# Kernel optimization log

Measured on AMD Instinct MI355X. Metric: run time of the kernel, lower is better.

The kernel has to match this reference:

```python
import jax, jax.numpy as jnp
import numpy as np

B, H, S, D = 4, 16, 2048, 128

def setup_inputs() -> dict:
    key = jax.random.key(0)
    kq, kk, kv = jax.random.split(key, 3)
    query = jax.random.normal(kq, (B, H, S, D), dtype=jnp.float32)
    k = jax.random.normal(kk, (B, H, S, D), dtype=jnp.float32)
    v = jax.random.normal(kv, (B, H, S, D), dtype=jnp.float32)
    # causal mask: True = masked (not attended), broadcastable to (B,H,S,S)
    mask = jnp.triu(jnp.ones((S, S), dtype=bool), k=1)[None, None, :, :]
    return {"query": query, "key": k, "value": v, "mask": mask}

def reference(query, key, value, mask):
    d_k = query.shape[-1]
    scale = 1.0 / np.sqrt(d_k).astype(np.float32)
    # scores: (B,H,Sq,Sk)
    scores = jnp.einsum('bhqd,bhkd->bhqk', query, key) * scale
    scores = jnp.where(mask, -jnp.inf, scores)
    attention_weights = jax.nn.softmax(scores, axis=-1)
    output = jnp.einsum('bhqk,bhkd->bhqd', attention_weights, value)
    return output, attention_weights
```

## Files before the change

### kernel.cpp

```cpp
#include <hip/hip_runtime.h>
#include <hip/hip_bf16.h>

#define B_ 4
#define H_ 16
#define S_ 2048
#define D_ 128

typedef unsigned short u16;
typedef unsigned int u32;

typedef __attribute__((ext_vector_type(8))) short bf16x8;
typedef __attribute__((ext_vector_type(4))) float f32x4;
typedef __attribute__((ext_vector_type(4))) unsigned short u16x4;

__device__ __forceinline__ float bf2f(u16 x) {
    return __uint_as_float(((u32)x) << 16);
}

__device__ __forceinline__ u16 f2bf(float f) {
    u32 u = __float_as_uint(f);
    u32 lsb = (u >> 16) & 1u;
    u += 0x7fffu + lsb;
    return (u16)(u >> 16);
}

#define LBAR() do {                                            \
    asm volatile("s_waitcnt lgkmcnt(0)" ::: "memory");         \
    __builtin_amdgcn_s_barrier();                              \
} while (0)

__global__ void detect_dtype_kernel(const u32* __restrict__ q, int* __restrict__ flag) {
    __shared__ int cnt;
    if (threadIdx.x == 0) cnt = 0;
    __syncthreads();
    int c = 0;
    for (int i = threadIdx.x; i < 4096; i += 256) {
        float lo = bf2f((u16)(q[i] & 0xffffu));
        if (!(fabsf(lo) <= 64.0f)) c++;
    }
    atomicAdd(&cnt, c);
    __syncthreads();
    if (threadIdx.x == 0) *flag = (cnt > 256) ? 1 : 0;
}

__global__ __launch_bounds__(256) void attn_bf16_kernel(
    const u16* __restrict__ Q, const u16* __restrict__ K, const u16* __restrict__ V,
    u16* __restrict__ Out, u16* __restrict__ W, const int* __restrict__ flag)
{
    if (*flag != 0) return;

    __shared__ float qs[D_];
    __shared__ float sc[S_];
    __shared__ float red[8];
    __shared__ float ot[512];

    const int tid = threadIdx.x;
    for (int idx = blockIdx.x; idx < B_ * H_ * S_; idx += (int)gridDim.x) {
        const int q   = idx & (S_ - 1);
        const int bh  = idx >> 11;
        const size_t rowQ = (size_t)idx * D_;
        const u16* Kb = K + (size_t)bh * S_ * D_;
        const u16* Vb = V + (size_t)bh * S_ * D_;
        const int nk = q + 1;
        const float scale = 0.08838834764831845f;

        if (tid < D_) qs[tid] = bf2f(Q[rowQ + tid]) * scale;
        __syncthreads();

        float lmax = -1e30f;
        for (int k = tid; k < nk; k += 256) {
            const uint4* K4 = reinterpret_cast<const uint4*>(Kb + (size_t)k * D_);
            float acc = 0.f;
            #pragma unroll
            for (int c = 0; c < D_ / 8; ++c) {
                uint4 u = K4[c];
                const int d = c * 8;
                acc += qs[d + 0] * bf2f((u16)(u.x & 0xffffu));
                acc += qs[d + 1] * bf2f((u16)(u.x >> 16));
                acc += qs[d + 2] * bf2f((u16)(u.y & 0xffffu));
                acc += qs[d + 3] * bf2f((u16)(u.y >> 16));
                acc += qs[d + 4] * bf2f((u16)(u.z & 0xffffu));
                acc += qs[d + 5] * bf2f((u16)(u.z >> 16));
                acc += qs[d + 6] * bf2f((u16)(u.w & 0xffffu));
                acc += qs[d + 7] * bf2f((u16)(u.w >> 16));
            }
            sc[k] = acc;
            lmax = fmaxf(lmax, acc);
        }

        #pragma unroll
        for (int off = 32; off > 0; off >>= 1)
            lmax = fmaxf(lmax, __shfl_down(lmax, off, 64));
        if ((tid & 63) == 0) red[tid >> 6] = lmax;
        __syncthreads();
        const float mx = fmaxf(fmaxf(red[0], red[1]), fmaxf(red[2], red[3]));

        float lsum = 0.f;
        for (int k = tid; k < nk; k += 256) {
            float e = __expf(sc[k] - mx);
            sc[k] = e;
            lsum += e;
        }
        #pragma unroll
        for (int off = 32; off > 0; off >>= 1)
            lsum += __shfl_down(lsum, off, 64);
        if ((tid & 63) == 0) red[4 + (tid >> 6)] = lsum;
        __syncthreads();
        const float rsum = 1.0f / (red[4] + red[5] + red[6] + red[7]);

        u32* Wrow2 = reinterpret_cast<u32*>(W + (size_t)idx * S_);
        for (int k2 = tid; k2 < S_ / 2; k2 += 256) {
            const int k0 = 2 * k2, k1 = 2 * k2 + 1;
            float w0 = (k0 < nk) ? sc[k0] * rsum : 0.f;
            float w1 = (k1 < nk) ? sc[k1] * rsum : 0.f;
            if (k0 < nk) sc[k0] = w0;
            if (k1 < nk) sc[k1] = w1;
            Wrow2[k2] = (u32)f2bf(w0) | ((u32)f2bf(w1) << 16);
        }
        __syncthreads();

        const int d2   = tid & 63;
        const int part = tid >> 6;
        const u32* V2 = reinterpret_cast<const u32*>(Vb);
        float a0 = 0.f, a1 = 0.f;
        for (int k = part; k < nk; k += 4) {
            const u32 u = V2[(size_t)k * (D_ / 2) + d2];
            const float w = sc[k];
            a0 += w * bf2f((u16)(u & 0xffffu));
            a1 += w * bf2f((u16)(u >> 16));
        }
        ot[part * D_ + 2 * d2]     = a0;
        ot[part * D_ + 2 * d2 + 1] = a1;
        __syncthreads();

        if (tid < D_) {
            const float o = ot[tid] + ot[D_ + tid] + ot[2 * D_ + tid] + ot[3 * D_ + tid];
            Out[rowQ + tid] = f2bf(o);
        }
        __syncthreads();
    }
}

__global__ __launch_bounds__(256) void split_qk_kernel(
    const float* __restrict__ Q, const float* __restrict__ K,
    u16* __restrict__ Qh, u16* __restrict__ Ql,
    u16* __restrict__ Kh, u16* __restrict__ Kl,
    const int* __restrict__ flag)
{
    if (*flag != 1) return;
    const float scale = 0.08838834764831845f;
    const int N4 = (B_ * H_ * S_ * D_) / 4;
    const float4* Q4 = reinterpret_cast<const float4*>(Q);
    const float4* K4 = reinterpret_cast<const float4*>(K);
    for (int g = blockIdx.x * 256 + threadIdx.x; g < N4; g += 2048 * 256) {
        {
            float4 v = Q4[g];
            float s0 = v.x * scale, s1 = v.y * scale, s2 = v.z * scale, s3 = v.w * scale;
            u16 h0 = f2bf(s0), h1 = f2bf(s1), h2 = f2bf(s2), h3 = f2bf(s3);
            u16x4 hv = {h0, h1, h2, h3};
            u16x4 lv = {f2bf(s0 - bf2f(h0)), f2bf(s1 - bf2f(h1)),
                        f2bf(s2 - bf2f(h2)), f2bf(s3 - bf2f(h3))};
            *reinterpret_cast<u16x4*>(&Qh[(size_t)4 * g]) = hv;
            *reinterpret_cast<u16x4*>(&Ql[(size_t)4 * g]) = lv;
        }
        {
            float4 v = K4[g];
            u16 h0 = f2bf(v.x), h1 = f2bf(v.y), h2 = f2bf(v.z), h3 = f2bf(v.w);
            u16x4 hv = {h0, h1, h2, h3};
            u16x4 lv = {f2bf(v.x - bf2f(h0)), f2bf(v.y - bf2f(h1)),
                        f2bf(v.z - bf2f(h2)), f2bf(v.w - bf2f(h3))};
            *reinterpret_cast<u16x4*>(&Kh[(size_t)4 * g]) = hv;
            *reinterpret_cast<u16x4*>(&Kl[(size_t)4 * g]) = lv;
        }
    }
}

__global__ __launch_bounds__(256) void transpose_v_kernel(
    const float* __restrict__ V, u16* __restrict__ VT, const int* __restrict__ flag)
{
    if (*flag != 1) return;
    __shared__ float ts[64 * 130];
    const int tid = threadIdx.x;
    const int bh = blockIdx.x >> 5;
    const int kt = blockIdx.x & 31;
    const int k0 = kt * 64;
    const float4* V4 = reinterpret_cast<const float4*>(V + ((size_t)bh * S_ + k0) * D_);
    #pragma unroll
    for (int it = 0; it < 8; ++it) {
        int g = tid + 256 * it;
        int r = g >> 5, c4 = g & 31;
        float4 v = V4[g];
        ts[r * 130 + 4 * c4 + 0] = v.x;
        ts[r * 130 + 4 * c4 + 1] = v.y;
        ts[r * 130 + 4 * c4 + 2] = v.z;
        ts[r * 130 + 4 * c4 + 3] = v.w;
    }
    __syncthreads();
    const int d = tid >> 1, kh2 = tid & 1;
    u16* dst = VT + (size_t)bh * (D_ * S_) + (size_t)d * S_ + k0 + 32 * kh2;
    #pragma unroll
    for (int jj = 0; jj < 4; ++jj) {
        bf16x8 o;
        #pragma unroll
        for (int j = 0; j < 8; ++j) {
            int k = 32 * kh2 + 8 * jj + j;
            o[j] = (short)f2bf(ts[k * 130 + d]);
        }
        *reinterpret_cast<bf16x8*>(&dst[8 * jj]) = o;
    }
}

#define ESTR 68

__global__ __launch_bounds__(256, 2) void attn_mfma_kernel(
    const u16* __restrict__ Qh, const u16* __restrict__ Ql,
    const u16* __restrict__ Kh, const u16* __restrict__ Kl,
    const u16* __restrict__ VT,
    float* __restrict__ Out, float* __restrict__ W, const int* __restrict__ flag)
{
    if (*flag != 1) return;

    __shared__ __align__(16) short qh_s[32 * 128];
    __shared__ __align__(16) short ql_s[32 * 128];
    __shared__ __align__(16) short kh_s[64 * 128];
    __shared__ __align__(16) short kl_s[64 * 128];
    __shared__ __align__(16) short vt_s[128 * 64];
    __shared__ __align__(16) float e_s[32 * ESTR];
    __shared__ float red2[2][32];
    __shared__ float rinv_s[32];

    const int tid = threadIdx.x;
    const int w   = tid >> 6;
    const int l   = tid & 63;
    const int l15 = l & 15;
    const int l4  = l >> 4;
    const int fq  = w >> 1;
    const int fk  = w & 1;

    const int bidx = blockIdx.x;
    const int bh   = bidx >> 6;
    const int qt   = 63 - (bidx & 63);
    const int q0   = qt << 5;
    const int nkt  = (q0 + 95) >> 6;

    const u16* QhB = Qh + ((size_t)bh * S_ + q0) * D_;
    const u16* QlB = Ql + ((size_t)bh * S_ + q0) * D_;
    const u16* KhB = Kh + (size_t)bh * S_ * D_;
    const u16* KlB = Kl + (size_t)bh * S_ * D_;
    const u16* VTB = VT + (size_t)bh * (size_t)D_ * S_;
    float* Ob = Out + ((size_t)bh * S_ + q0) * D_;
    float* Wb = W + ((size_t)bh * S_ + q0) * (size_t)S_;

    #pragma unroll
    for (int it = 0; it < 2; ++it) {
        int g = tid + 256 * it;
        int r = g >> 4, ch = g & 15;
        bf16x8 a = *reinterpret_cast<const bf16x8*>(&QhB[(size_t)r * D_ + 8 * ch]);
        bf16x8 b = *reinterpret_cast<const bf16x8*>(&QlB[(size_t)r * D_ + 8 * ch]);
        int li = r * 128 + ((8 * ch) ^ ((r & 7) << 3));
        *reinterpret_cast<bf16x8*>(&qh_s[li]) = a;
        *reinterpret_cast<bf16x8*>(&ql_s[li]) = b;
    }

    const int qrow = 16 * fq + l15;
    const int qx   = (qrow & 7) << 3;
    const int col0 = 8 * l4;

    f32x4 oacc[4];
    #pragma unroll
    for (int nb = 0; nb < 4; ++nb) { oacc[nb] = {0.f, 0.f, 0.f, 0.f}; }
    float rs[4] = {0.f, 0.f, 0.f, 0.f};

    bf16x8 rkh[4], rkl[4], rvt[4];
    {
        #pragma unroll
        for (int it = 0; it < 4; ++it) {
            int g = tid + 256 * it;
            rkh[it] = *reinterpret_cast<const bf16x8*>(&KhB[(size_t)(g >> 4) * D_ + 8 * (g & 15)]);
            rkl[it] = *reinterpret_cast<const bf16x8*>(&KlB[(size_t)(g >> 4) * D_ + 8 * (g & 15)]);
            rvt[it] = *reinterpret_cast<const bf16x8*>(&VTB[(size_t)(g >> 3) * S_ + 8 * (g & 7)]);
        }
    }

    for (int kt = 0; kt < nkt; ++kt) {
        const int k0 = kt << 6;

        #pragma unroll
        for (int it = 0; it < 4; ++it) {
            int g = tid + 256 * it;
            int r = g >> 4, ch = g & 15;
            int li = r * 128 + ((8 * ch) ^ ((r & 7) << 3));
            *reinterpret_cast<bf16x8*>(&kh_s[li]) = rkh[it];
            *reinterpret_cast<bf16x8*>(&kl_s[li]) = rkl[it];
            int d = g >> 3, c8 = g & 7;
            *reinterpret_cast<bf16x8*>(&vt_s[d * 64 + 8 * (c8 ^ (d & 7))]) = rvt[it];
        }
        LBAR();

        if (kt + 1 < nkt) {
            const int kn = k0 + 64;
            #pragma unroll
            for (int it = 0; it < 4; ++it) {
                int g = tid + 256 * it;
                rkh[it] = *reinterpret_cast<const bf16x8*>(&KhB[(size_t)(kn + (g >> 4)) * D_ + 8 * (g & 15)]);
                rkl[it] = *reinterpret_cast<const bf16x8*>(&KlB[(size_t)(kn + (g >> 4)) * D_ + 8 * (g & 15)]);
                rvt[it] = *reinterpret_cast<const bf16x8*>(&VTB[(size_t)(g >> 3) * S_ + kn + 8 * (g & 7)]);
            }
        }

        f32x4 acc2[2];
        acc2[0] = {0.f, 0.f, 0.f, 0.f};
        acc2[1] = {0.f, 0.f, 0.f, 0.f};
        __builtin_amdgcn_s_setprio(1);
        #pragma unroll
        for (int nb = 0; nb < 2; ++nb) {
            const int krow = 32 * fk + 16 * nb + l15;
            const int kx   = (krow & 7) << 3;
            #pragma unroll
            for (int ks = 0; ks < 4; ++ks) {
                int ca = 32 * ks + col0;
                bf16x8 aH = *reinterpret_cast<const bf16x8*>(&qh_s[qrow * 128 + (ca ^ qx)]);
                bf16x8 aL = *reinterpret_cast<const bf16x8*>(&ql_s[qrow * 128 + (ca ^ qx)]);
                bf16x8 bH = *reinterpret_cast<const bf16x8*>(&kh_s[krow * 128 + (ca ^ kx)]);
                bf16x8 bL = *reinterpret_cast<const bf16x8*>(&kl_s[krow * 128 + (ca ^ kx)]);
                acc2[nb] = __builtin_amdgcn_mfma_f32_16x16x32_bf16(aH, bH, acc2[nb], 0, 0, 0);
                acc2[nb] = __builtin_amdgcn_mfma_f32_16x16x32_bf16(aH, bL, acc2[nb], 0, 0, 0);
                acc2[nb] = __builtin_amdgcn_mfma_f32_16x16x32_bf16(aL, bH, acc2[nb], 0, 0, 0);
            }
        }
        __builtin_amdgcn_s_setprio(0);

        #pragma unroll
        for (int nb = 0; nb < 2; ++nb) {
            #pragma unroll
            for (int i = 0; i < 4; ++i) {
                int row = 16 * fq + 4 * l4 + i;
                int col = 32 * fk + 16 * nb + l15;
                float e = 0.f;
                if (k0 + col <= q0 + row) e = __expf(acc2[nb][i]);
                rs[i] += e;
                e_s[row * ESTR + col] = e;
            }
        }
        LBAR();

        #pragma unroll
        for (int t = 0; t < 2; ++t) {
            int idx = tid + 256 * t;
            int row = idx >> 4, c4 = idx & 15;
            f32x4 wv = *reinterpret_cast<const f32x4*>(&e_s[row * ESTR + 4 * c4]);
            *reinterpret_cast<f32x4*>(Wb + (size_t)row * S_ + k0 + 4 * c4) = wv;
        }

        #pragma unroll
        for (int ks2 = 0; ks2 < 2; ++ks2) {
            bf16x8 aP;
            {
                const float* pr = &e_s[(16 * fq + l15) * ESTR + 32 * ks2 + col0];
                float4 p0 = *reinterpret_cast<const float4*>(pr);
                float4 p1 = *reinterpret_cast<const float4*>(pr + 4);
                aP[0] = (short)f2bf(p0.x); aP[1] = (short)f2bf(p0.y);
                aP[2] = (short)f2bf(p0.z); aP[3] = (short)f2bf(p0.w);
                aP[4] = (short)f2bf(p1.x); aP[5] = (short)f2bf(p1.y);
                aP[6] = (short)f2bf(p1.z); aP[7] = (short)f2bf(p1.w);
            }
            __builtin_amdgcn_s_setprio(1);
            #pragma unroll
            for (int nb = 0; nb < 4; ++nb) {
                int dcol = 64 * fk + 16 * nb + l15;
                bf16x8 bV = *reinterpret_cast<const bf16x8*>(
                    &vt_s[dcol * 64 + 8 * ((4 * ks2 + l4) ^ (dcol & 7))]);
                oacc[nb] = __builtin_amdgcn_mfma_f32_16x16x32_bf16(aP, bV, oacc[nb], 0, 0, 0);
            }
            __builtin_amdgcn_s_setprio(0);
        }
        LBAR();
    }

    #pragma unroll
    for (int i = 0; i < 4; ++i) {
        float v = rs[i];
        v += __shfl_xor(v, 1, 64);
        v += __shfl_xor(v, 2, 64);
        v += __shfl_xor(v, 4, 64);
        v += __shfl_xor(v, 8, 64);
        if (l15 == 0) red2[fk][16 * fq + 4 * l4 + i] = v;
    }
    __syncthreads();
    if (tid < 32) rinv_s[tid] = 1.0f / (red2[0][tid] + red2[1][tid]);
    __syncthreads();

    #pragma unroll
    for (int nb = 0; nb < 4; ++nb) {
        #pragma unroll
        for (int i = 0; i < 4; ++i) {
            int row = 16 * fq + 4 * l4 + i;
            int col = 64 * fk + 16 * nb + l15;
            Ob[(size_t)row * D_ + col] = oacc[nb][i] * rinv_s[row];
        }
    }

    {
        const int kend = nkt << 6;
        f32x4* W4 = reinterpret_cast<f32x4*>(Wb);
        const f32x4 z4 = {0.f, 0.f, 0.f, 0.f};
        for (int g = tid; g < 32 * (S_ / 4); g += 256) {
            const int row = g >> 9;
            const int c4  = g & 511;
            const size_t off = (size_t)row * (S_ / 4) + c4;
            if ((c4 << 2) < kend) {
                f32x4 wv = W4[off];
                const float inv = rinv_s[row];
                wv.x *= inv; wv.y *= inv; wv.z *= inv; wv.w *= inv;
                W4[off] = wv;
            } else {
                __builtin_nontemporal_store(z4, &W4[off]);
            }
        }
    }
}

#define BQ 32
#define BK 64
#define LSTR 33
#define FESTR 68

__device__ __forceinline__ void dot4(float& a, const float4& x, const float4& y) {
    a = fmaf(x.x, y.x, a); a = fmaf(x.y, y.y, a);
    a = fmaf(x.z, y.z, a); a = fmaf(x.w, y.w, a);
}
__device__ __forceinline__ void fma4(float4& a, float s, const float4& b) {
    a.x = fmaf(s, b.x, a.x); a.y = fmaf(s, b.y, a.y);
    a.z = fmaf(s, b.z, a.z); a.w = fmaf(s, b.w, a.w);
}

__global__ __launch_bounds__(256) void attn_f32_tiled(
    const float* __restrict__ Q, const float* __restrict__ K, const float* __restrict__ V,
    float* __restrict__ Out, float* __restrict__ W, const int* __restrict__ flag)
{
    if (*flag != 1) return;

    __shared__ float4 qs4[BQ * LSTR];
    __shared__ float4 kv4[BK * LSTR];
    __shared__ __align__(16) float e_s[BQ * FESTR];
    __shared__ float rsum_s[BQ];
    __shared__ float rinv_s[BQ];

    const int tid  = threadIdx.x;
    const int bidx = blockIdx.x;
    const int bh   = bidx >> 6;
    const int qt   = 63 - (bidx & 63);
    const int q0   = qt << 5;
    const int nkt  = ((q0 + BQ - 1) >> 6) + 1;
    const float scale = 0.08838834764831845f;

    const float* Kb = K + (size_t)bh * (S_ * D_);
    const float* Vb = V + (size_t)bh * (S_ * D_);
    const float* Qb = Q + ((size_t)bh * S_ + q0) * D_;
    float* Ob = Out + ((size_t)bh * S_ + q0) * D_;
    float* Wb = W + ((size_t)bh * S_ + q0) * (size_t)S_;

    const int rgq = tid >> 4;
    const int cgq = tid & 15;
    const int rg = tid >> 4;
    const int cg = tid & 15;

    {
        const float4* Qg = reinterpret_cast<const float4*>(Qb);
        #pragma unroll
        for (int t = 0; t < 4; ++t) {
            const int g = tid + 256 * t;
            qs4[(g >> 5) * LSTR + (g & 31)] = Qg[g];
        }
        const float4* Kg = reinterpret_cast<const float4*>(Kb);
        #pragma unroll
        for (int t = 0; t < 8; ++t) {
            const int g = tid + 256 * t;
            kv4[(g >> 5) * LSTR + (g & 31)] = Kg[g];
        }
    }
    __syncthreads();

    float4 o4[2][2] = {};
    float rsf[2] = {0.f, 0.f};

    for (int kt = 0; kt < nkt; ++kt) {
        const int k0 = kt << 6;
        const bool more = (kt + 1 < nkt);

        float4 vreg[8];
        {
            const float4* Vg = reinterpret_cast<const float4*>(Vb) + (size_t)k0 * 32;
            #pragma unroll
            for (int t = 0; t < 8; ++t) vreg[t] = Vg[tid + 256 * t];
        }

        float acc[2][4] = {};
        {
            const int qb0 = (rgq * 2 + 0) * LSTR;
            const int qb1 = (rgq * 2 + 1) * LSTR;
            const int kb0 = (cgq +  0) * LSTR;
            const int kb1 = (cgq + 16) * LSTR;
            const int kb2 = (cgq + 32) * LSTR;
            const int kb3 = (cgq + 48) * LSTR;
            #pragma unroll 4
            for (int d4 = 0; d4 < 32; ++d4) {
                const float4 qv0 = qs4[qb0 + d4];
                const float4 qv1 = qs4[qb1 + d4];
                const float4 kv0 = kv4[kb0 + d4];
                const float4 kv1 = kv4[kb1 + d4];
                const float4 kv2 = kv4[kb2 + d4];
                const float4 kv3 = kv4[kb3 + d4];
                dot4(acc[0][0], qv0, kv0); dot4(acc[0][1], qv0, kv1);
                dot4(acc[0][2], qv0, kv2); dot4(acc[0][3], qv0, kv3);
                dot4(acc[1][0], qv1, kv0); dot4(acc[1][1], qv1, kv1);
                dot4(acc[1][2], qv1, kv2); dot4(acc[1][3], qv1, kv3);
            }
        }

        #pragma unroll
        for (int i = 0; i < 2; ++i) {
            const int r  = rgq * 2 + i;
            const int qg = q0 + r;
            float* Wrow = Wb + (size_t)r * S_ + k0;
            #pragma unroll
            for (int j = 0; j < 4; ++j) {
                const int kc = cgq + 16 * j;
                const float e = (k0 + kc <= qg) ? __expf(acc[i][j] * scale) : 0.0f;
                rsf[i] += e;
                e_s[r * FESTR + kc] = e;
                Wrow[kc] = e;
            }
        }
        __syncthreads();

        #pragma unroll
        for (int t = 0; t < 8; ++t) {
            const int g = tid + 256 * t;
            kv4[(g >> 5) * LSTR + (g & 31)] = vreg[t];
        }
        float4 kreg[8];
        if (more) {
            const float4* Kg = reinterpret_cast<const float4*>(Kb) + (size_t)(k0 + BK) * 32;
            #pragma unroll
            for (int t = 0; t < 8; ++t) kreg[t] = Kg[tid + 256 * t];
        }
        __syncthreads();

        {
            const int eb0 = (rg * 2 + 0) * FESTR;
            const int eb1 = (rg * 2 + 1) * FESTR;
            #pragma unroll 2
            for (int kk = 0; kk < BK; kk += 4) {
                const float4 e0 = *reinterpret_cast<const float4*>(&e_s[eb0 + kk]);
                const float4 e1 = *reinterpret_cast<const float4*>(&e_s[eb1 + kk]);
                const float ea[4] = {e0.x, e0.y, e0.z, e0.w};
                const float eb[4] = {e1.x, e1.y, e1.z, e1.w};
                #pragma unroll
                for (int t = 0; t < 4; ++t) {
                    const float4 v0 = kv4[(kk + t) * LSTR + cg];
                    const float4 v1 = kv4[(kk + t) * LSTR + 16 + cg];
                    fma4(o4[0][0], ea[t], v0);
                    fma4(o4[0][1], ea[t], v1);
                    fma4(o4[1][0], eb[t], v0);
                    fma4(o4[1][1], eb[t], v1);
                }
            }
        }

        if (more) {
            __syncthreads();
            #pragma unroll
            for (int t = 0; t < 8; ++t) {
                const int g = tid + 256 * t;
                kv4[(g >> 5) * LSTR + (g & 31)] = kreg[t];
            }
            __syncthreads();
        }
    }

    #pragma unroll
    for (int i = 0; i < 2; ++i) {
        float v = rsf[i];
        v += __shfl_xor(v, 8, 64);
        v += __shfl_xor(v, 4, 64);
        v += __shfl_xor(v, 2, 64);
        v += __shfl_xor(v, 1, 64);
        if (cgq == 0) rsum_s[rgq * 2 + i] = v;
    }
    __syncthreads();
    if (tid < BQ) rinv_s[tid] = 1.0f / rsum_s[tid];
    __syncthreads();

    #pragma unroll
    for (int i = 0; i < 2; ++i) {
        const int r = rg * 2 + i;
        const float inv = rinv_s[r];
        float4 a = o4[i][0];
        a.x *= inv; a.y *= inv; a.z *= inv; a.w *= inv;
        float4 b = o4[i][1];
        b.x *= inv; b.y *= inv; b.z *= inv; b.w *= inv;
        float4* Orow = reinterpret_cast<float4*>(Ob + (size_t)r * D_);
        Orow[cg]      = a;
        Orow[16 + cg] = b;
    }

    {
        const int kend = nkt << 6;
        float4* W4 = reinterpret_cast<float4*>(Wb);
        for (int g = tid; g < BQ * (S_ / 4); g += 256) {
            const int row = g >> 9;
            const int c4  = g & 511;
            const size_t off = (size_t)row * (S_ / 4) + c4;
            if ((c4 << 2) < kend) {
                float4 wv = W4[off];
                const float inv = rinv_s[row];
                wv.x *= inv; wv.y *= inv; wv.z *= inv; wv.w *= inv;
                W4[off] = wv;
            } else {
                W4[off] = make_float4(0.f, 0.f, 0.f, 0.f);
            }
        }
    }
}

extern "C" void kernel_launch(void* const* d_in, const int* in_sizes, int n_in,
                              void* d_out, int out_size, void* d_ws, size_t ws_size,
                              hipStream_t stream) {
    int* flag = (int*)d_ws;

    detect_dtype_kernel<<<dim3(1), dim3(256), 0, stream>>>((const u32*)d_in[0], flag);

    {
        const u16* Q = (const u16*)d_in[0];
        const u16* K = (const u16*)d_in[1];
        const u16* V = (const u16*)d_in[2];
        u16* Out = (u16*)d_out;
        u16* Wp  = Out + (size_t)B_ * H_ * S_ * D_;
        attn_bf16_kernel<<<dim3(2048), dim3(256), 0, stream>>>(Q, K, V, Out, Wp, flag);
    }

    const size_t PLSZ = (size_t)B_ * H_ * S_ * D_;
    const size_t NEED = 256 + 5 * PLSZ * sizeof(u16);
    float* OutF = (float*)d_out;
    float* WF   = OutF + PLSZ;

    if (ws_size >= NEED) {
        u16* base = (u16*)((char*)d_ws + 256);
        u16* Qh = base;
        u16* Ql = Qh + PLSZ;
        u16* Kh = Ql + PLSZ;
        u16* Kl = Kh + PLSZ;
        u16* VTp = Kl + PLSZ;
        split_qk_kernel<<<dim3(2048), dim3(256), 0, stream>>>(
            (const float*)d_in[0], (const float*)d_in[1], Qh, Ql, Kh, Kl, flag);
        transpose_v_kernel<<<dim3(2048), dim3(256), 0, stream>>>(
            (const float*)d_in[2], VTp, flag);
        attn_mfma_kernel<<<dim3(B_ * H_ * (S_ / 32)), dim3(256), 0, stream>>>(
            Qh, Ql, Kh, Kl, VTp, OutF, WF, flag);
    } else {
        attn_f32_tiled<<<dim3(B_ * H_ * (S_ / 32)), dim3(256), 0, stream>>>(
            (const float*)d_in[0], (const float*)d_in[1], (const float*)d_in[2],
            OutF, WF, flag);
    }
}
```

Measured before the change: 1.918 ms.

## Use two-pass softmax to write normalized weights once instead of rescaling

```diff
diff --git a/kernel.cpp b/kernel.cpp
--- a/kernel.cpp
+++ b/kernel.cpp
@@ -266,115 +266,72 @@
     const int qx   = (qrow & 7) << 3;
     const int col0 = 8 * l4;
 
-    f32x4 oacc[4];
-    #pragma unroll
-    for (int nb = 0; nb < 4; ++nb) { oacc[nb] = {0.f, 0.f, 0.f, 0.f}; }
     float rs[4] = {0.f, 0.f, 0.f, 0.f};
 
-    bf16x8 rkh[4], rkl[4], rvt[4];
     {
+        bf16x8 rkh[4], rkl[4];
         #pragma unroll
         for (int it = 0; it < 4; ++it) {
             int g = tid + 256 * it;
             rkh[it] = *reinterpret_cast<const bf16x8*>(&KhB[(size_t)(g >> 4) * D_ + 8 * (g & 15)]);
             rkl[it] = *reinterpret_cast<const bf16x8*>(&KlB[(size_t)(g >> 4) * D_ + 8 * (g & 15)]);
-            rvt[it] = *reinterpret_cast<const bf16x8*>(&VTB[(size_t)(g >> 3) * S_ + 8 * (g & 7)]);
-        }
-    }
-
-    for (int kt = 0; kt < nkt; ++kt) {
-        const int k0 = kt << 6;
-
-        #pragma unroll
-        for (int it = 0; it < 4; ++it) {
-            int g = tid + 256 * it;
-            int r = g >> 4, ch = g & 15;
-            int li = r * 128 + ((8 * ch) ^ ((r & 7) << 3));
-            *reinterpret_cast<bf16x8*>(&kh_s[li]) = rkh[it];
-            *reinterpret_cast<bf16x8*>(&kl_s[li]) = rkl[it];
-            int d = g >> 3, c8 = g & 7;
-            *reinterpret_cast<bf16x8*>(&vt_s[d * 64 + 8 * (c8 ^ (d & 7))]) = rvt[it];
-        }
-        LBAR();
-
-        if (kt + 1 < nkt) {
-            const int kn = k0 + 64;
+        }
+
+        for (int kt = 0; kt < nkt; ++kt) {
+            const int k0 = kt << 6;
             #pragma unroll
             for (int it = 0; it < 4; ++it) {
                 int g = tid + 256 * it;
-                rkh[it] = *reinterpret_cast<const bf16x8*>(&KhB[(size_t)(kn + (g >> 4)) * D_ + 8 * (g & 15)]);
-                rkl[it] = *reinterpret_cast<const bf16x8*>(&KlB[(size_t)(kn + (g >> 4)) * D_ + 8 * (g & 15)]);
-                rvt[it] = *reinterpret_cast<const bf16x8*>(&VTB[(size_t)(g >> 3) * S_ + kn + 8 * (g & 7)]);
-            }
-        }
-
-        f32x4 acc2[2];
-        acc2[0] = {0.f, 0.f, 0.f, 0.f};
-        acc2[1] = {0.f, 0.f, 0.f, 0.f};
-        __builtin_amdgcn_s_setprio(1);
-        #pragma unroll
-        for (int nb = 0; nb < 2; ++nb) {
-            const int krow = 32 * fk + 16 * nb + l15;
-            const int kx   = (krow & 7) << 3;
-            #pragma unroll
-            for (int ks = 0; ks < 4; ++ks) {
-                int ca = 32 * ks + col0;
-                bf16x8 aH = *reinterpret_cast<const bf16x8*>(&qh_s[qrow * 128 + (ca ^ qx)]);
-                bf16x8 aL = *reinterpret_cast<const bf16x8*>(&ql_s[qrow * 128 + (ca ^ qx)]);
-                bf16x8 bH = *reinterpret_cast<const bf16x8*>(&kh_s[krow * 128 + (ca ^ kx)]);
-                bf16x8 bL = *reinterpret_cast<const bf16x8*>(&kl_s[krow * 128 + (ca ^ kx)]);
-                acc2[nb] = __builtin_amdgcn_mfma_f32_16x16x32_bf16(aH, bH, acc2[nb], 0, 0, 0);
-                acc2[nb] = __builtin_amdgcn_mfma_f32_16x16x32_bf16(aH, bL, acc2[nb], 0, 0, 0);
-                acc2[nb] = __builtin_amdgcn_mfma_f32_16x16x32_bf16(aL, bH, acc2[nb], 0, 0, 0);
-            }
-        }
-        __builtin_amdgcn_s_setprio(0);
-
-        #pragma unroll
-        for (int nb = 0; nb < 2; ++nb) {
-            #pragma unroll
-            for (int i = 0; i < 4; ++i) {
-                int row = 16 * fq + 4 * l4 + i;
-                int col = 32 * fk + 16 * nb + l15;
-                float e = 0.f;
-                if (k0 + col <= q0 + row) e = __expf(acc2[nb][i]);
-                rs[i] += e;
-                e_s[row * ESTR + col] = e;
-            }
-        }
-        LBAR();
-
-        #pragma unroll
-        for (int t = 0; t < 2; ++t) {
-            int idx = tid + 256 * t;
-            int row = idx >> 4, c4 = idx & 15;
-            f32x4 wv = *reinterpret_cast<const f32x4*>(&e_s[row * ESTR + 4 * c4]);
-            *reinterpret_cast<f32x4*>(Wb + (size_t)row * S_ + k0 + 4 * c4) = wv;
-        }
-
-        #pragma unroll
-        for (int ks2 = 0; ks2 < 2; ++ks2) {
-            bf16x8 aP;
-            {
-                const float* pr = &e_s[(16 * fq + l15) * ESTR + 32 * ks2 + col0];
-                float4 p0 = *reinterpret_cast<const float4*>(pr);
-                float4 p1 = *reinterpret_cast<const float4*>(pr + 4);
-                aP[0] = (short)f2bf(p0.x); aP[1] = (short)f2bf(p0.y);
-                aP[2] = (short)f2bf(p0.z); aP[3] = (short)f2bf(p0.w);
-                aP[4] = (short)f2bf(p1.x); aP[5] = (short)f2bf(p1.y);
-                aP[6] = (short)f2bf(p1.z); aP[7] = (short)f2bf(p1.w);
-            }
+                int r = g >> 4, ch = g & 15;
+                int li = r * 128 + ((8 * ch) ^ ((r & 7) << 3));
+                *reinterpret_cast<bf16x8*>(&kh_s[li]) = rkh[it];
+                *reinterpret_cast<bf16x8*>(&kl_s[li]) = rkl[it];
+            }
+            LBAR();
+
+            if (kt + 1 < nkt) {
+                const int kn = k0 + 64;
+                #pragma unroll
+                for (int it = 0; it < 4; ++it) {
+                    int g = tid + 256 * it;
+                    rkh[it] = *reinterpret_cast<const bf16x8*>(&KhB[(size_t)(kn + (g >> 4)) * D_ + 8 * (g & 15)]);
+                    rkl[it] = *reinterpret_cast<const bf16x8*>(&KlB[(size_t)(kn + (g >> 4)) * D_ + 8 * (g & 15)]);
+                }
+            }
+
+            f32x4 acc2[2];
+            acc2[0] = {0.f, 0.f, 0.f, 0.f};
+            acc2[1] = {0.f, 0.f, 0.f, 0.f};
             __builtin_amdgcn_s_setprio(1);
             #pragma unroll
-            for (int nb = 0; nb < 4; ++nb) {
-                int dcol = 64 * fk + 16 * nb + l15;
-                bf16x8 bV = *reinterpret_cast<const bf16x8*>(
-                    &vt_s[dcol * 64 + 8 * ((4 * ks2 + l4) ^ (dcol & 7))]);
-                oacc[nb] = __builtin_amdgcn_mfma_f32_16x16x32_bf16(aP, bV, oacc[nb], 0, 0, 0);
+            for (int nb = 0; nb < 2; ++nb) {
+                const int krow = 32 * fk + 16 * nb + l15;
+                const int kx   = (krow & 7) << 3;
+                #pragma unroll
+                for (int ks = 0; ks < 4; ++ks) {
+                    int ca = 32 * ks + col0;
+                    bf16x8 aH = *reinterpret_cast<const bf16x8*>(&qh_s[qrow * 128 + (ca ^ qx)]);
+                    bf16x8 aL = *reinterpret_cast<const bf16x8*>(&ql_s[qrow * 128 + (ca ^ qx)]);
+                    bf16x8 bH = *reinterpret_cast<const bf16x8*>(&kh_s[krow * 128 + (ca ^ kx)]);
+                    bf16x8 bL = *reinterpret_cast<const bf16x8*>(&kl_s[krow * 128 + (ca ^ kx)]);
+                    acc2[nb] = __builtin_amdgcn_mfma_f32_16x16x32_bf16(aH, bH, acc2[nb], 0, 0, 0);
+                    acc2[nb] = __builtin_amdgcn_mfma_f32_16x16x32_bf16(aH, bL, acc2[nb], 0, 0, 0);
+                    acc2[nb] = __builtin_amdgcn_mfma_f32_16x16x32_bf16(aL, bH, acc2[nb], 0, 0, 0);
+                }
             }
             __builtin_amdgcn_s_setprio(0);
-        }
-        LBAR();
+
+            #pragma unroll
+            for (int nb = 0; nb < 2; ++nb) {
+                #pragma unroll
+                for (int i = 0; i < 4; ++i) {
+                    int row = 16 * fq + 4 * l4 + i;
+                    int col = 32 * fk + 16 * nb + l15;
+                    if (k0 + col <= q0 + row) rs[i] += __expf(acc2[nb][i]);
+                }
+            }
+            LBAR();
+        }
     }
 
     #pragma unroll
@@ -390,32 +347,138 @@
     if (tid < 32) rinv_s[tid] = 1.0f / (red2[0][tid] + red2[1][tid]);
     __syncthreads();
 
+    float rinvr[4];
+    #pragma unroll
+    for (int i = 0; i < 4; ++i) rinvr[i] = rinv_s[16 * fq + 4 * l4 + i];
+
+    f32x4 oacc[4];
+    #pragma unroll
+    for (int nb = 0; nb < 4; ++nb) { oacc[nb] = {0.f, 0.f, 0.f, 0.f}; }
+
+    {
+        bf16x8 rkh[4], rkl[4], rvt[4];
+        #pragma unroll
+        for (int it = 0; it < 4; ++it) {
+            int g = tid + 256 * it;
+            rkh[it] = *reinterpret_cast<const bf16x8*>(&KhB[(size_t)(g >> 4) * D_ + 8 * (g & 15)]);
+            rkl[it] = *reinterpret_cast<const bf16x8*>(&KlB[(size_t)(g >> 4) * D_ + 8 * (g & 15)]);
+            rvt[it] = *reinterpret_cast<const bf16x8*>(&VTB[(size_t)(g >> 3) * S_ + 8 * (g & 7)]);
+        }
+
+        for (int kt = 0; kt < nkt; ++kt) {
+            const int k0 = kt << 6;
+            #pragma unroll
+            for (int it = 0; it < 4; ++it) {
+                int g = tid + 256 * it;
+                int r = g >> 4, ch = g & 15;
+                int li = r * 128 + ((8 * ch) ^ ((r & 7) << 3));
+                *reinterpret_cast<bf16x8*>(&kh_s[li]) = rkh[it];
+                *reinterpret_cast<bf16x8*>(&kl_s[li]) = rkl[it];
+                int d = g >> 3, c8 = g & 7;
+                *reinterpret_cast<bf16x8*>(&vt_s[d * 64 + 8 * (c8 ^ (d & 7))]) = rvt[it];
+            }
+            LBAR();
+
+            if (kt + 1 < nkt) {
+                const int kn = k0 + 64;
+                #pragma unroll
+                for (int it = 0; it < 4; ++it) {
+                    int g = tid + 256 * it;
+                    rkh[it] = *reinterpret_cast<const bf16x8*>(&KhB[(size_t)(kn + (g >> 4)) * D_ + 8 * (g & 15)]);
+                    rkl[it] = *reinterpret_cast<const bf16x8*>(&KlB[(size_t)(kn + (g >> 4)) * D_ + 8 * (g & 15)]);
+                    rvt[it] = *reinterpret_cast<const bf16x8*>(&VTB[(size_t)(g >> 3) * S_ + kn + 8 * (g & 7)]);
+                }
+            }
+
+            f32x4 acc2[2];
+            acc2[0] = {0.f, 0.f, 0.f, 0.f};
+            acc2[1] = {0.f, 0.f, 0.f, 0.f};
+            __builtin_amdgcn_s_setprio(1);
+            #pragma unroll
+            for (int nb = 0; nb < 2; ++nb) {
+                const int krow = 32 * fk + 16 * nb + l15;
+                const int kx   = (krow & 7) << 3;
+                #pragma unroll
+                for (int ks = 0; ks < 4; ++ks) {
+                    int ca = 32 * ks + col0;
+                    bf16x8 aH = *reinterpret_cast<const bf16x8*>(&qh_s[qrow * 128 + (ca ^ qx)]);
+                    bf16x8 aL = *reinterpret_cast<const bf16x8*>(&ql_s[qrow * 128 + (ca ^ qx)]);
+                    bf16x8 bH = *reinterpret_cast<const bf16x8*>(&kh_s[krow * 128 + (ca ^ kx)]);
+                    bf16x8 bL = *reinterpret_cast<const bf16x8*>(&kl_s[krow * 128 + (ca ^ kx)]);
+                    acc2[nb] = __builtin_amdgcn_mfma_f32_16x16x32_bf16(aH, bH, acc2[nb], 0, 0, 0);
+                    acc2[nb] = __builtin_amdgcn_mfma_f32_16x16x32_bf16(aH, bL, acc2[nb], 0, 0, 0);
+                    acc2[nb] = __builtin_amdgcn_mfma_f32_16x16x32_bf16(aL, bH, acc2[nb], 0, 0, 0);
+                }
+            }
+            __builtin_amdgcn_s_setprio(0);
+
+            #pragma unroll
+            for (int nb = 0; nb < 2; ++nb) {
+                #pragma unroll
+                for (int i = 0; i < 4; ++i) {
+                    int row = 16 * fq + 4 * l4 + i;
+                    int col = 32 * fk + 16 * nb + l15;
+                    float e = 0.f;
+                    if (k0 + col <= q0 + row) e = __expf(acc2[nb][i]) * rinvr[i];
+                    e_s[row * ESTR + col] = e;
+                }
+            }
+            LBAR();
+
+            #pragma unroll
+            for (int t = 0; t < 2; ++t) {
+                int idx = tid + 256 * t;
+                int row = idx >> 4, c4 = idx & 15;
+                f32x4 wv = *reinterpret_cast<const f32x4*>(&e_s[row * ESTR + 4 * c4]);
+                __builtin_nontemporal_store(wv,
+                    reinterpret_cast<f32x4*>(Wb + (size_t)row * S_ + k0 + 4 * c4));
+            }
+
+            #pragma unroll
+            for (int ks2 = 0; ks2 < 2; ++ks2) {
+                bf16x8 aP;
+                {
+                    const float* pr = &e_s[(16 * fq + l15) * ESTR + 32 * ks2 + col0];
+                    float4 p0 = *reinterpret_cast<const float4*>(pr);
+                    float4 p1 = *reinterpret_cast<const float4*>(pr + 4);
+                    aP[0] = (short)f2bf(p0.x); aP[1] = (short)f2bf(p0.y);
+                    aP[2] = (short)f2bf(p0.z); aP[3] = (short)f2bf(p0.w);
+                    aP[4] = (short)f2bf(p1.x); aP[5] = (short)f2bf(p1.y);
+                    aP[6] = (short)f2bf(p1.z); aP[7] = (short)f2bf(p1.w);
+                }
+                __builtin_amdgcn_s_setprio(1);
+                #pragma unroll
+                for (int nb = 0; nb < 4; ++nb) {
+                    int dcol = 64 * fk + 16 * nb + l15;
+                    bf16x8 bV = *reinterpret_cast<const bf16x8*>(
+                        &vt_s[dcol * 64 + 8 * ((4 * ks2 + l4) ^ (dcol & 7))]);
+                    oacc[nb] = __builtin_amdgcn_mfma_f32_16x16x32_bf16(aP, bV, oacc[nb], 0, 0, 0);
+                }
+                __builtin_amdgcn_s_setprio(0);
+            }
+            LBAR();
+        }
+    }
+
     #pragma unroll
     for (int nb = 0; nb < 4; ++nb) {
         #pragma unroll
         for (int i = 0; i < 4; ++i) {
             int row = 16 * fq + 4 * l4 + i;
             int col = 64 * fk + 16 * nb + l15;
-            Ob[(size_t)row * D_ + col] = oacc[nb][i] * rinv_s[row];
+            Ob[(size_t)row * D_ + col] = oacc[nb][i];
         }
     }
 
     {
-        const int kend = nkt << 6;
+        const int kend4 = nkt << 4;
         f32x4* W4 = reinterpret_cast<f32x4*>(Wb);
         const f32x4 z4 = {0.f, 0.f, 0.f, 0.f};
-        for (int g = tid; g < 32 * (S_ / 4); g += 256) {
-            const int row = g >> 9;
-            const int c4  = g & 511;
-            const size_t off = (size_t)row * (S_ / 4) + c4;
-            if ((c4 << 2) < kend) {
-                f32x4 wv = W4[off];
-                const float inv = rinv_s[row];
-                wv.x *= inv; wv.y *= inv; wv.z *= inv; wv.w *= inv;
-                W4[off] = wv;
-            } else {
-                __builtin_nontemporal_store(z4, &W4[off]);
-            }
+        const int zc = 512 - kend4;
+        for (int g = tid; g < 32 * zc; g += 256) {
+            const int row = g / zc;
+            const int c4  = kend4 + (g - row * zc);
+            __builtin_nontemporal_store(z4, &W4[(size_t)row * 512 + c4]);
         }
     }
 }
```

Result: faster. 1.799 ms (-6.2%).
